# Kernel tuning notes

Hardware: AMD Instinct MI355X
Metric: run time of the kernel (lower is better)

## Reference

```python
import jax, jax.numpy as jnp
import numpy as np

B, N, E, DIN = 2048, 38, 4, 9
H0, H1, L0 = 256, 256, 512
EPS = 1e-5
_mask_np = np.ones((N, DIN), np.float32)
_mask_np[np.arange(0, N, 2), :] = 0.0
MASK = jnp.asarray(_mask_np)  # (N, DIN); masked rows zeroed


def _bn_relu(h, g, b):
    # h: (B, N, 1, D); BatchNorm2d(N) normalizes over (batch, H=1, W=D) per node channel
    mu = jnp.mean(h, axis=(0, 2, 3), keepdims=True)
    var = jnp.var(h, axis=(0, 2, 3), keepdims=True)  # biased var, as torch BN
    h = (h - mu) * jax.lax.rsqrt(var + EPS) * g[None, :, None, None] + b[None, :, None, None]
    return jax.nn.relu(h)


def _gconv(adj, nodes, Ws, bs, We, be):
    # adj: (B, E, N, N); nodes: (B, N, 1, Din)
    out = Ws.shape[0]
    hs = nodes @ Ws.T + bs  # self term: (B, N, 1, out)
    m = (nodes @ We.T + be).reshape(nodes.shape[0], N, out, E)
    hr = jnp.einsum('bemn,bnce->bmc', adj, m)  # relational aggregation
    return hs + hr[:, :, None, :]


def _forward(adj, x, cWs0, cbs0, cWe0, cbe0, cg0, cb0, cWs1, cbs1, cWe1, cbe1, cg1, cb1, lW0, lb0, lg0, lbb0, fW, fb):
    masked_x = MASK * x
    h = masked_x[:, :, None, :]
    h = _bn_relu(_gconv(adj, h, cWs0, cbs0, cWe0, cbe0), cg0, cb0)
    h = _bn_relu(_gconv(adj, h, cWs1, cbs1, cWe1, cbe1), cg1, cb1)
    h = _bn_relu(h @ lW0.T + lb0, lg0, lbb0)
    h = (h @ fW.T + fb)[:, :, 0, :]  # (B, N, 2*DIN)
    s_logits, t = h[..., :DIN], h[..., DIN:]
    s = jax.nn.sigmoid(s_logits)
    out = masked_x + (1.0 - MASK) * (x + t) * s
    logdet = jnp.sum(jax.nn.log_sigmoid(s_logits).reshape(x.shape[0], -1), axis=1)
    return out, logdet


def setup_inputs() -> dict:
    key = jax.random.key(0)
    ks = jax.random.split(key, 8)
    rn = lambda k, shape: jax.random.normal(ks[k], shape, jnp.float32) * 0.1
    return {
        'adj': jax.random.uniform(ks[0], (B, E, N, N), jnp.float32),
        'x': jax.random.normal(ks[1], (B, N, DIN), jnp.float32),
        'cWs0': rn(2, (H0, DIN)), 'cbs0': jnp.zeros((H0,), jnp.float32),
        'cWe0': rn(3, (H0 * E, DIN)), 'cbe0': jnp.zeros((H0 * E,), jnp.float32),
        'cg0': jnp.ones((N,), jnp.float32), 'cb0': jnp.zeros((N,), jnp.float32),
        'cWs1': rn(4, (H1, H0)), 'cbs1': jnp.zeros((H1,), jnp.float32),
        'cWe1': rn(5, (H1 * E, H0)), 'cbe1': jnp.zeros((H1 * E,), jnp.float32),
        'cg1': jnp.ones((N,), jnp.float32), 'cb1': jnp.zeros((N,), jnp.float32),
        'lW0': rn(6, (L0, H1)), 'lb0': jnp.zeros((L0,), jnp.float32),
        'lg0': jnp.ones((N,), jnp.float32), 'lbb0': jnp.zeros((N,), jnp.float32),
        'fW': rn(7, (2 * DIN, L0)), 'fb': jnp.zeros((2 * DIN,), jnp.float32),
    }


def reference(adj, x, cWs0, cbs0, cWe0, cbe0, cg0, cb0, cWs1, cbs1, cWe1, cbe1, cg1, cb1, lW0, lb0, lg0, lbb0, fW, fb):
    return _forward(adj, x, cWs0, cbs0, cWe0, cbe0, cg0, cb0, cWs1, cbs1, cWe1, cbe1, cg1, cb1, lW0, lb0, lg0, lbb0, fW, fb)
```

## Files before the change

kernel.cpp:

```cpp
#include <hip/hip_runtime.h>
#include <hip/hip_bf16.h>
#include <math.h>

#define B_   2048
#define N_   38
#define E_   4
#define DIN_ 9
#define H0_  256
#define H1_  256
#define L0_  512
#define M_   (B_ * N_)

typedef short bf16x8 __attribute__((ext_vector_type(8)));
typedef float f32x4 __attribute__((ext_vector_type(4)));

struct __align__(8) bf4 { __hip_bfloat16 x, y, z, w; };

__device__ __forceinline__ float b2f(unsigned short u) {
  return __uint_as_float((unsigned)u << 16);
}
__device__ __forceinline__ unsigned short f2b(float f) {
  __hip_bfloat16 h = __float2bfloat16(f);
  return *(unsigned short*)&h;
}
__device__ __forceinline__ float4 ld4v(const __hip_bfloat16* p) {
  bf4 v = *(const bf4*)p;
  return make_float4(__bfloat162float(v.x), __bfloat162float(v.y),
                     __bfloat162float(v.z), __bfloat162float(v.w));
}
__device__ __forceinline__ void st4v(__hip_bfloat16* p, float4 v) {
  bf4 o;
  o.x = __float2bfloat16(v.x); o.y = __float2bfloat16(v.y);
  o.z = __float2bfloat16(v.z); o.w = __float2bfloat16(v.w);
  *(bf4*)p = o;
}

static __device__ __forceinline__ float selc(const float4 v, int j) {
  return (j == 0) ? v.x : ((j == 1) ? v.y : ((j == 2) ? v.z : v.w));
}

__device__ __forceinline__ void fma_tile12(const float* __restrict__ zr, float4 w,
                                           float (&acc)[4][12]) {
#pragma unroll
  for (int l4 = 0; l4 < 3; ++l4) {
    float4 zv = *(const float4*)&zr[l4 * 4];
#pragma unroll
    for (int j = 0; j < 4; ++j) {
      float wj = selc(w, j);
      acc[j][l4 * 4 + 0] = fmaf(zv.x, wj, acc[j][l4 * 4 + 0]);
      acc[j][l4 * 4 + 1] = fmaf(zv.y, wj, acc[j][l4 * 4 + 1]);
      acc[j][l4 * 4 + 2] = fmaf(zv.z, wj, acc[j][l4 * 4 + 2]);
      acc[j][l4 * 4 + 3] = fmaf(zv.w, wj, acc[j][l4 * 4 + 3]);
    }
  }
}

__global__ void k_zero(float* __restrict__ p) { p[threadIdx.x] = 0.f; }

__global__ void k_build_w0(const float* __restrict__ Ws, const float* __restrict__ We,
                           float* __restrict__ WT) {
  int i = blockIdx.x * 256 + threadIdx.x;
  if (i >= 45 * 256) return;
  int r = i / 256, c = i % 256;
  float v;
  if (r < 9) v = Ws[c * 9 + r];
  else { int rr = r - 9; int e = rr / 9, f = rr % 9; v = We[(c * 4 + e) * 9 + f]; }
  WT[i] = v;
}

__global__ void k_build_wb1(const float* __restrict__ Ws, const float* __restrict__ We,
                            unsigned short* __restrict__ WT) {
  int i = blockIdx.x * 256 + threadIdx.x;
  if (i >= 256 * 1280) return;
  int c = i / 1280, k = i % 1280;
  float v;
  if (k < 256) v = Ws[c * 256 + k];
  else { int kk = k - 256; int e = kk >> 8, f = kk & 255; v = We[(c * 4 + e) * 256 + f]; }
  WT[i] = f2b(v);
}

__global__ void k_build_wl(const float* __restrict__ W, unsigned short* __restrict__ WT) {
  int i = blockIdx.x * 256 + threadIdx.x;
  if (i >= 512 * 256) return;
  WT[i] = f2b(W[i]);
}

__global__ void k_build_wf(const float* __restrict__ W, unsigned short* __restrict__ WT) {
  int i = blockIdx.x * 256 + threadIdx.x;
  if (i >= 32 * 512) return;
  int r = i / 512, k = i % 512;
  WT[i] = f2b(r < 18 ? W[r * 512 + k] : 0.f);
}

__global__ __launch_bounds__(256) void k_gconv0(
    const float* __restrict__ adj, const float* __restrict__ x,
    const float* __restrict__ WT, const float* __restrict__ bs,
    const float* __restrict__ be, __hip_bfloat16* __restrict__ g) {
  __shared__ __align__(16) float adjF[E_ * N_ * N_];
  __shared__ __align__(16) float xc[45 * 48];
  __shared__ __align__(16) float arow[E_ * 48];
  const int b = blockIdx.x, tid = threadIdx.x;
  const size_t abase = (size_t)b * (E_ * N_ * N_);
  for (int i = tid; i < E_ * N_ * N_; i += 256) adjF[i] = adj[abase + i];
  for (int i = tid; i < N_ * DIN_; i += 256) {
    int n = i / DIN_;
    float v = x[(size_t)b * (N_ * DIN_) + i];
    xc[(i % DIN_) * 48 + n] = (n & 1) ? v : 0.f;
  }
  __syncthreads();
  for (int i = tid; i < E_ * N_; i += 256) {
    int e = i / N_, m = i % N_;
    const float* ar = &adjF[(e * N_ + m) * N_];
    float s = 0.f;
    for (int n = 0; n < N_; ++n) s += ar[n];
    arow[e * 48 + m] = s;
  }
  for (int i = tid; i < 36 * N_; i += 256) {
    int m = i % N_, ef = i / N_;
    int e = ef / 9, f = ef % 9;
    const float* ar = &adjF[(e * N_ + m) * N_];
    float s = 0.f;
    for (int n = 0; n < N_; ++n) s += ar[n] * xc[f * 48 + n];
    xc[(9 + ef) * 48 + m] = s;
  }
  __syncthreads();
  const int cg = tid & 63, mg = tid >> 6;
  const int c0 = cg * 4, mb = mg * 12;
  float acc[4][12];
#pragma unroll
  for (int j = 0; j < 4; ++j) {
    float bsv = bs[c0 + j];
    float b0 = be[(c0 + j) * 4 + 0], b1 = be[(c0 + j) * 4 + 1];
    float b2 = be[(c0 + j) * 4 + 2], b3 = be[(c0 + j) * 4 + 3];
#pragma unroll
    for (int l = 0; l < 12; ++l) {
      int m = mb + l;
      acc[j][l] = bsv + arow[0 * 48 + m] * b0 + arow[1 * 48 + m] * b1 +
                  arow[2 * 48 + m] * b2 + arow[3 * 48 + m] * b3;
    }
  }
  for (int k = 0; k < 45; ++k) {
    float4 w = *(const float4*)&WT[k * 256 + c0];
    fma_tile12(&xc[k * 48 + mb], w, acc);
  }
#pragma unroll
  for (int l = 0; l < 12; ++l) {
    int m = mb + l;
    if (m < N_) {
      float4 o; o.x = acc[0][l]; o.y = acc[1][l]; o.z = acc[2][l]; o.w = acc[3][l];
      st4v(&g[((size_t)b * N_ + m) * H0_ + c0], o);
    }
  }
}

__global__ __launch_bounds__(256) void k_stats(const __hip_bfloat16* __restrict__ g, int C,
                                               float* __restrict__ st) {
  int n = blockIdx.x, s = blockIdx.y, tid = threadIdx.x;
  int C4 = C >> 2;
  float sum = 0.f, sq = 0.f;
  int per = 64 * C4;
  for (int j = tid; j < per; j += 256) {
    int bb = (s << 6) + j / C4, cc = j % C4;
    float4 v = ld4v(&g[((size_t)(bb * N_ + n) * C4 + cc) * 4]);
    sum += v.x + v.y + v.z + v.w;
    sq += v.x * v.x + v.y * v.y + v.z * v.z + v.w * v.w;
  }
  for (int off = 32; off; off >>= 1) {
    sum += __shfl_down(sum, off);
    sq += __shfl_down(sq, off);
  }
  __shared__ float rs[4], rq[4];
  int w = tid >> 6, l = tid & 63;
  if (!l) { rs[w] = sum; rq[w] = sq; }
  __syncthreads();
  if (!tid) {
    float S = 0.f, Q = 0.f;
    for (int i = 0; i < 4; ++i) { S += rs[i]; Q += rq[i]; }
    atomicAdd(&st[n * 2], S);
    atomicAdd(&st[n * 2 + 1], Q);
  }
}

#define ADJS 72
#define ZBS2 264

__global__ __launch_bounds__(512, 4) void k_gc1f(
    const float* __restrict__ adj, const unsigned short* __restrict__ g0,
    const unsigned short* __restrict__ Wb1, const float* __restrict__ bs,
    const float* __restrict__ be, const float* __restrict__ st,
    const float* __restrict__ gam, const float* __restrict__ bet,
    unsigned short* __restrict__ h2) {
  __shared__ __align__(16) unsigned short adjB[4 * 38 * ADJS];
  __shared__ __align__(16) unsigned short zB[48 * ZBS2];
  __shared__ float arowS[4 * 48];
  __shared__ float aS[40], bS[40];
  __shared__ float lbias[256];
  const int b = blockIdx.x, tid = threadIdx.x;
  for (int i = tid; i < 4 * 38 * ADJS / 8; i += 512) ((uint4*)adjB)[i] = make_uint4(0, 0, 0, 0);
  if (tid < 40) {
    int n = tid < 38 ? tid : 37;
    const float cnt = 2048.f * 256.f;
    float mu = st[n * 2] / cnt;
    float var = st[n * 2 + 1] / cnt - mu * mu;
    float a = rsqrtf(var + 1e-5f) * gam[n];
    aS[tid] = a;
    bS[tid] = bet[n] - mu * a;
  }
  if (tid >= 64 && tid < 320) lbias[tid - 64] = bs[tid - 64];
  __syncthreads();
  for (int i = tid; i < 4 * 38 * 38; i += 512) {
    int em = i / 38, n = i % 38;
    adjB[em * ADJS + n] = f2b(adj[(size_t)b * 5776 + i]);
  }
  __syncthreads();
  if (tid < 152) {
    int e = tid / 38, m = tid % 38;
    float s = 0.f;
    for (int n = 0; n < 38; ++n) s += b2f(adjB[(e * 38 + m) * ADJS + n]);
    arowS[e * 48 + m] = s;
  }
  const int w = tid >> 6, L = tid & 63;
  const int lrow = L & 15, quad = L >> 4;
  bf16x8 hfr[2][2];
#pragma unroll
  for (int ft = 0; ft < 2; ++ft) {
    const int fcol = (w * 2 + ft) * 16 + lrow;
#pragma unroll
    for (int kk = 0; kk < 2; ++kk) {
#pragma unroll
      for (int j = 0; j < 8; ++j) {
        int n = kk * 32 + quad * 8 + j;
        int nc = n < 38 ? n : 37;
        float v = b2f(g0[((size_t)b * 38 + n) * 256 + fcol]);
        v = fmaxf(fmaf(v, aS[nc], bS[nc]), 0.f);
        hfr[ft][kk][j] = (short)f2b(v);
      }
    }
  }
  f32x4 acc[3][2];
#pragma unroll
  for (int mt = 0; mt < 3; ++mt) {
    acc[mt][0] = (f32x4){0.f, 0.f, 0.f, 0.f};
    acc[mt][1] = (f32x4){0.f, 0.f, 0.f, 0.f};
  }
#pragma unroll 1
  for (int e = 0; e < 4; ++e) {
    f32x4 za[3][2];
#pragma unroll
    for (int mt = 0; mt < 3; ++mt) {
      za[mt][0] = (f32x4){0.f, 0.f, 0.f, 0.f};
      za[mt][1] = (f32x4){0.f, 0.f, 0.f, 0.f};
    }
#pragma unroll
    for (int kk = 0; kk < 2; ++kk) {
#pragma unroll
      for (int mt = 0; mt < 3; ++mt) {
        int m = mt * 16 + lrow;
        int mc = m < 38 ? m : 37;
        bf16x8 aa = *(const bf16x8*)&adjB[(e * 38 + mc) * ADJS + kk * 32 + quad * 8];
        za[mt][0] = __builtin_amdgcn_mfma_f32_16x16x32_bf16(aa, hfr[0][kk], za[mt][0], 0, 0, 0);
        za[mt][1] = __builtin_amdgcn_mfma_f32_16x16x32_bf16(aa, hfr[1][kk], za[mt][1], 0, 0, 0);
      }
    }
    __syncthreads();
#pragma unroll
    for (int mt = 0; mt < 3; ++mt)
#pragma unroll
      for (int ft = 0; ft < 2; ++ft)
#pragma unroll
        for (int reg = 0; reg < 4; ++reg)
          zB[(mt * 16 + quad * 4 + reg) * ZBS2 + (w * 2 + ft) * 16 + lrow] =
              f2b(za[mt][ft][reg]);
    __syncthreads();
    if (e == 0) {
#pragma unroll 2
      for (int kc = 0; kc < 8; ++kc) {
        bf16x8 bb0 = *(const bf16x8*)&Wb1[(size_t)(w * 32 + lrow) * 1280 + kc * 32 + quad * 8];
        bf16x8 bb1 = *(const bf16x8*)&Wb1[(size_t)(w * 32 + 16 + lrow) * 1280 + kc * 32 + quad * 8];
#pragma unroll
        for (int mt = 0; mt < 3; ++mt) {
          int m = mt * 16 + lrow;
          int mc = m < 38 ? m : 37;
          float a = aS[mc], bo = bS[mc];
          uint4 u = *(const uint4*)&g0[((size_t)b * 38 + mc) * 256 + kc * 32 + quad * 8];
          bf16x8 af;
          unsigned* up = (unsigned*)&u;
#pragma unroll
          for (int h = 0; h < 4; ++h) {
            float lo = fmaxf(fmaf(b2f((unsigned short)(up[h] & 0xffff)), a, bo), 0.f);
            float hi = fmaxf(fmaf(b2f((unsigned short)(up[h] >> 16)), a, bo), 0.f);
            af[h * 2] = (short)f2b(lo);
            af[h * 2 + 1] = (short)f2b(hi);
          }
          acc[mt][0] = __builtin_amdgcn_mfma_f32_16x16x32_bf16(af, bb0, acc[mt][0], 0, 0, 0);
          acc[mt][1] = __builtin_amdgcn_mfma_f32_16x16x32_bf16(af, bb1, acc[mt][1], 0, 0, 0);
        }
      }
    }
#pragma unroll 2
    for (int kcl = 0; kcl < 8; ++kcl) {
      const int kbase = 256 + e * 256 + kcl * 32;
      bf16x8 bb0 = *(const bf16x8*)&Wb1[(size_t)(w * 32 + lrow) * 1280 + kbase + quad * 8];
      bf16x8 bb1 = *(const bf16x8*)&Wb1[(size_t)(w * 32 + 16 + lrow) * 1280 + kbase + quad * 8];
#pragma unroll
      for (int mt = 0; mt < 3; ++mt) {
        bf16x8 af = *(const bf16x8*)&zB[(mt * 16 + lrow) * ZBS2 + kcl * 32 + quad * 8];
        acc[mt][0] = __builtin_amdgcn_mfma_f32_16x16x32_bf16(af, bb0, acc[mt][0], 0, 0, 0);
        acc[mt][1] = __builtin_amdgcn_mfma_f32_16x16x32_bf16(af, bb1, acc[mt][1], 0, 0, 0);
      }
    }
  }
#pragma unroll
  for (int mt = 0; mt < 3; ++mt) {
#pragma unroll
    for (int reg = 0; reg < 4; ++reg) {
      const int m = mt * 16 + quad * 4 + reg;
      if (m < N_) {
        float a0 = arowS[0 * 48 + m], a1 = arowS[1 * 48 + m];
        float a2 = arowS[2 * 48 + m], a3 = arowS[3 * 48 + m];
#pragma unroll
        for (int nt = 0; nt < 2; ++nt) {
          const int col = w * 32 + nt * 16 + lrow;
          float4 bev = *(const float4*)&be[col * 4];
          float v = acc[mt][nt][reg] + lbias[col] +
                    a0 * bev.x + a1 * bev.y + a2 * bev.z + a3 * bev.w;
          h2[((size_t)b * N_ + m) * 256 + col] = f2b(v);
        }
      }
    }
  }
}

__global__ __launch_bounds__(256) void k_mm(
    const unsigned short* __restrict__ A0, const unsigned short* __restrict__ Bw,
    const float* __restrict__ bias, unsigned short* __restrict__ Cout,
    int m_base, int kChunks, int sA0, int Cstride) {
  __shared__ __align__(16) unsigned short lA[64 * 32];
  __shared__ __align__(16) unsigned short lB[256 * 32];
  __shared__ float lbias[256];
  const int t = threadIdx.x;
  const int tileM = blockIdx.x, n_base = blockIdx.y * 256;
  const int K = kChunks * 32;
  for (int i = t; i < 256; i += 256) lbias[i] = bias[n_base + i];

  const int w = t >> 6, L = t & 63;
  const int lrow = L & 15, quad = L >> 4;
  const int srow = t >> 2, sseg = (t & 3) * 8;

  f32x4 acc[4][4];
#pragma unroll
  for (int mt = 0; mt < 4; ++mt)
#pragma unroll
    for (int nt = 0; nt < 4; ++nt) acc[mt][nt] = (f32x4){0.f, 0.f, 0.f, 0.f};

  for (int ki = 0; ki < kChunks; ++ki) {
    {
      const unsigned short* gp =
          A0 + (size_t)(m_base + tileM * 64 + srow) * sA0 + ki * 32 + sseg;
      __builtin_amdgcn_global_load_lds(
          (const __attribute__((address_space(1))) void*)gp,
          (__attribute__((address_space(3))) void*)(lA + w * 512), 16, 0, 0);
    }
#pragma unroll
    for (int r = 0; r < 4; ++r) {
      const unsigned short* gp = Bw + (size_t)(n_base + r * 64 + srow) * K + ki * 32 + sseg;
      __builtin_amdgcn_global_load_lds(
          (const __attribute__((address_space(1))) void*)gp,
          (__attribute__((address_space(3))) void*)(lB + r * 2048 + w * 512), 16, 0, 0);
    }
    __syncthreads();
    bf16x8 af[4], bfr[4];
#pragma unroll
    for (int mt = 0; mt < 4; ++mt)
      af[mt] = *(const bf16x8*)&lA[(mt * 16 + lrow) * 32 + quad * 8];
#pragma unroll
    for (int nt = 0; nt < 4; ++nt)
      bfr[nt] = *(const bf16x8*)&lB[(w * 64 + nt * 16 + lrow) * 32 + quad * 8];
#pragma unroll
    for (int mt = 0; mt < 4; ++mt)
#pragma unroll
      for (int nt = 0; nt < 4; ++nt)
        acc[mt][nt] = __builtin_amdgcn_mfma_f32_16x16x32_bf16(af[mt], bfr[nt], acc[mt][nt], 0, 0, 0);
    __syncthreads();
  }
#pragma unroll
  for (int mt = 0; mt < 4; ++mt) {
#pragma unroll
    for (int reg = 0; reg < 4; ++reg) {
      const size_t r_loc = (size_t)(tileM * 64 + mt * 16 + quad * 4 + reg);
#pragma unroll
      for (int nt = 0; nt < 4; ++nt) {
        const int col = w * 64 + nt * 16 + lrow;
        Cout[r_loc * Cstride + n_base + col] = f2b(acc[mt][nt][reg] + lbias[col]);
      }
    }
  }
}

__global__ __launch_bounds__(256) void k_prep2(
    unsigned short* __restrict__ g, const float* __restrict__ st,
    const float* __restrict__ gam, const float* __restrict__ bet) {
  size_t i = (size_t)blockIdx.x * 256 + threadIdx.x;
  int n = (int)((i >> 5) % N_);
  const float cnt = 2048.f * 256.f;
  float mu = st[n * 2] / cnt;
  float var = st[n * 2 + 1] / cnt - mu * mu;
  float a = rsqrtf(var + 1e-5f) * gam[n];
  float bb = bet[n] - mu * a;
  uint4 u = *((const uint4*)g + i);
  uint4 o;
  unsigned* up = (unsigned*)&u;
  unsigned* op = (unsigned*)&o;
#pragma unroll
  for (int j = 0; j < 4; ++j) {
    float lo = b2f((unsigned short)(up[j] & 0xffff));
    float hi = b2f((unsigned short)(up[j] >> 16));
    lo = fmaxf(fmaf(lo, a, bb), 0.f);
    hi = fmaxf(fmaf(hi, a, bb), 0.f);
    op[j] = (unsigned)f2b(lo) | ((unsigned)f2b(hi) << 16);
  }
  *((uint4*)g + i) = o;
}

__global__ __launch_bounds__(256) void k_final(
    const unsigned short* __restrict__ g2, const float* __restrict__ x,
    const unsigned short* __restrict__ Wfb, const float* __restrict__ fb,
    const float* __restrict__ st, const float* __restrict__ gam,
    const float* __restrict__ bet, float* __restrict__ out, int b_off) {
  __shared__ __align__(16) unsigned short hA[48 * 520];
  __shared__ float lgS[48 * 20];
  __shared__ float aS[N_], bS[N_], fbS[20], red[4];
  const int b = b_off + blockIdx.x, tid = threadIdx.x;
  const int bl = blockIdx.x;
  if (tid < N_) {
    const float cnt = 2048.f * 512.f;
    float mu = st[tid * 2] / cnt;
    float var = st[tid * 2 + 1] / cnt - mu * mu;
    float a = rsqrtf(var + 1e-5f) * gam[tid];
    aS[tid] = a;
    bS[tid] = bet[tid] - mu * a;
  }
  if (tid >= 64 && tid < 82) fbS[tid - 64] = fb[tid - 64];
  __syncthreads();
  for (int i = tid; i < N_ * 64; i += 256) {
    int n = i >> 6, seg = (i & 63) * 8;
    uint4 u = *(const uint4*)&g2[((size_t)bl * N_ + n) * 512 + seg];
    float a = aS[n], bb = bS[n];
    float v[8];
    v[0] = b2f((unsigned short)(u.x & 0xffff)); v[1] = b2f((unsigned short)(u.x >> 16));
    v[2] = b2f((unsigned short)(u.y & 0xffff)); v[3] = b2f((unsigned short)(u.y >> 16));
    v[4] = b2f((unsigned short)(u.z & 0xffff)); v[5] = b2f((unsigned short)(u.z >> 16));
    v[6] = b2f((unsigned short)(u.w & 0xffff)); v[7] = b2f((unsigned short)(u.w >> 16));
#pragma unroll
    for (int j = 0; j < 8; ++j) v[j] = fmaxf(fmaf(v[j], a, bb), 0.f);
    uint4 o;
    o.x = (unsigned)f2b(v[0]) | ((unsigned)f2b(v[1]) << 16);
    o.y = (unsigned)f2b(v[2]) | ((unsigned)f2b(v[3]) << 16);
    o.z = (unsigned)f2b(v[4]) | ((unsigned)f2b(v[5]) << 16);
    o.w = (unsigned)f2b(v[6]) | ((unsigned)f2b(v[7]) << 16);
    *(uint4*)&hA[n * 520 + seg] = o;
  }
  for (int i = tid; i < 10 * 64; i += 256) {
    int n = 38 + (i >> 6), seg = (i & 63) * 8;
    *(uint4*)&hA[n * 520 + seg] = make_uint4(0, 0, 0, 0);
  }
  __syncthreads();
  const int w = tid >> 6, L = tid & 63;
  const int lrow = L & 15, quad = L >> 4;
  if (w < 3) {
    f32x4 acc0 = (f32x4){0.f, 0.f, 0.f, 0.f}, acc1 = (f32x4){0.f, 0.f, 0.f, 0.f};
#pragma unroll
    for (int ki = 0; ki < 16; ++ki) {
      bf16x8 af = *(const bf16x8*)&hA[(w * 16 + lrow) * 520 + ki * 32 + quad * 8];
      bf16x8 b0 = *(const bf16x8*)&Wfb[(size_t)lrow * 512 + ki * 32 + quad * 8];
      bf16x8 b1 = *(const bf16x8*)&Wfb[(size_t)(16 + lrow) * 512 + ki * 32 + quad * 8];
      acc0 = __builtin_amdgcn_mfma_f32_16x16x32_bf16(af, b0, acc0, 0, 0, 0);
      acc1 = __builtin_amdgcn_mfma_f32_16x16x32_bf16(af, b1, acc1, 0, 0, 0);
    }
#pragma unroll
    for (int reg = 0; reg < 4; ++reg) {
      int m = w * 16 + quad * 4 + reg;
      if (m < N_) {
        lgS[m * 20 + lrow] = acc0[reg] + fbS[lrow];
        if (lrow < 2) lgS[m * 20 + 16 + lrow] = acc1[reg] + fbS[16 + lrow];
      }
    }
  }
  __syncthreads();
  float ls = 0.f;
  for (int ii = tid; ii < 342; ii += 256) {
    int mm = ii / 9, d = ii % 9;
    float sl = lgS[mm * 20 + d];
    float tv = lgS[mm * 20 + 9 + d];
    float xv = x[((size_t)b * N_ + mm) * 9 + d];
    float sg = 1.f / (1.f + expf(-sl));
    float o = (mm & 1) ? xv : (xv + tv) * sg;
    out[((size_t)b * N_ + mm) * 9 + d] = o;
    ls += (sl >= 0.f) ? -log1pf(expf(-sl)) : (sl - log1pf(expf(sl)));
  }
#pragma unroll
  for (int off = 32; off; off >>= 1) ls += __shfl_down(ls, off);
  if (L == 0) red[w] = ls;
  __syncthreads();
  if (tid == 0) out[(size_t)B_ * 342 + b] = red[0] + red[1] + red[2] + red[3];
}

extern "C" void kernel_launch(void* const* d_in, const int* in_sizes, int n_in,
                              void* d_out, int out_size, void* d_ws, size_t ws_size,
                              hipStream_t stream) {
  (void)in_sizes; (void)n_in; (void)out_size;
  const float* adj  = (const float*)d_in[0];
  const float* x    = (const float*)d_in[1];
  const float* cWs0 = (const float*)d_in[2];
  const float* cbs0 = (const float*)d_in[3];
  const float* cWe0 = (const float*)d_in[4];
  const float* cbe0 = (const float*)d_in[5];
  const float* cg0  = (const float*)d_in[6];
  const float* cb0  = (const float*)d_in[7];
  const float* cWs1 = (const float*)d_in[8];
  const float* cbs1 = (const float*)d_in[9];
  const float* cWe1 = (const float*)d_in[10];
  const float* cbe1 = (const float*)d_in[11];
  const float* cg1  = (const float*)d_in[12];
  const float* cb1  = (const float*)d_in[13];
  const float* lW0  = (const float*)d_in[14];
  const float* lb0  = (const float*)d_in[15];
  const float* lg0  = (const float*)d_in[16];
  const float* lbb0 = (const float*)d_in[17];
  const float* fW   = (const float*)d_in[18];
  const float* fb   = (const float*)d_in[19];
  float* out = (float*)d_out;

  char* p = (char*)d_ws;
  float* stats = (float*)p;                     p += 1024;
  float* wt0   = (float*)p;                     p += 45 * 256 * 4;
  unsigned short* Wfb = (unsigned short*)p;     p += 32 * 512 * 2;
  unsigned short* Wb1 = (unsigned short*)p;     p += 256 * 1280 * 2;
  unsigned short* Wl  = (unsigned short*)p;     p += 512 * 256 * 2;
  unsigned short* buf1 = (unsigned short*)p;    p += (size_t)M_ * 256 * 2;
  unsigned short* buf3 = (unsigned short*)p;    p += (size_t)M_ * 256 * 2;
  unsigned short* g2 = (unsigned short*)p;
  const size_t fixed = (size_t)((char*)g2 - (char*)d_ws);
  const bool full = ws_size >= fixed + (size_t)M_ * 512 * 2;

  k_zero<<<1, 256, 0, stream>>>(stats);
  k_build_w0<<<45, 256, 0, stream>>>(cWs0, cWe0, wt0);
  k_build_wb1<<<1280, 256, 0, stream>>>(cWs1, cWe1, Wb1);
  k_build_wl<<<512, 256, 0, stream>>>(lW0, Wl);
  k_build_wf<<<64, 256, 0, stream>>>(fW, Wfb);

  k_gconv0<<<2048, 256, 0, stream>>>(adj, x, wt0, cbs0, cbe0, (__hip_bfloat16*)buf1);
  k_stats<<<dim3(38, 32), 256, 0, stream>>>((const __hip_bfloat16*)buf1, 256, stats);

  k_gc1f<<<2048, 512, 0, stream>>>(adj, buf1, Wb1, cbs1, cbe1, stats, cg0, cb0, buf3);
  k_stats<<<dim3(38, 32), 256, 0, stream>>>((const __hip_bfloat16*)buf3, 256, stats + 76);

  k_prep2<<<(M_ * 256 / 8 + 255) / 256, 256, 0, stream>>>(buf3, stats + 76, cg1, cb1);

  if (full) {
    k_mm<<<dim3(M_ / 64, 2), 256, 0, stream>>>(buf3, Wl, lb0, g2, 0, 8, 256, 512);
    k_stats<<<dim3(38, 32), 256, 0, stream>>>((const __hip_bfloat16*)g2, 512, stats + 152);
    k_final<<<2048, 256, 0, stream>>>(g2, x, Wfb, fb, stats + 152, lg0, lbb0, out, 0);
  } else {
    for (int h = 0; h < 2; ++h) {
      k_mm<<<dim3(M_ / 128, 2), 256, 0, stream>>>(buf3, Wl, lb0, g2, h * (M_ / 2), 8, 256, 512);
      k_stats<<<dim3(38, 16), 256, 0, stream>>>((const __hip_bfloat16*)g2, 512, stats + 152);
    }
    for (int h = 0; h < 2; ++h) {
      k_mm<<<dim3(M_ / 128, 2), 256, 0, stream>>>(buf3, Wl, lb0, g2, h * (M_ / 2), 8, 256, 512);
      k_final<<<1024, 256, 0, stream>>>(g2, x, Wfb, fb, stats + 152, lg0, lbb0, out, h * 1024);
    }
  }
}
```

Measured before the change: 540.1 us.

## Reorder layer-1 gconv as feature GEMM first, then per-batch adjacency aggregation

Replaces the fused per-batch gconv1 kernel, which aggregated adjacency times h and then multiplied by the weights, with a large dense GEMM that first projects the normalized features onto a combined weight matrix (self plus 4 edge blocks, 1280 outputs). A separate kernel then multiplies the adjacency by the projected features per edge type and adds the self term and biases. BN-ReLU on layer 0 now runs as a separate in-place pass, and the linear layer uses a new 128x256 tile GEMM with 512 threads. The change also drops the fallback for a small workspace, so it assumes enough workspace for the 1280-wide intermediate. That intermediate adds global memory traffic in exchange for better MFMA utilization.

```diff
diff --git a/kernel.cpp b/kernel.cpp
--- a/kernel.cpp
+++ b/kernel.cpp
@@ -68,14 +68,14 @@
   WT[i] = v;
 }
 
-__global__ void k_build_wb1(const float* __restrict__ Ws, const float* __restrict__ We,
-                            unsigned short* __restrict__ WT) {
+__global__ void k_build_wbig(const float* __restrict__ Ws, const float* __restrict__ We,
+                             unsigned short* __restrict__ WT) {
   int i = blockIdx.x * 256 + threadIdx.x;
-  if (i >= 256 * 1280) return;
-  int c = i / 1280, k = i % 1280;
+  if (i >= 1280 * 256) return;
+  int j = i / 256, f = i % 256;
   float v;
-  if (k < 256) v = Ws[c * 256 + k];
-  else { int kk = k - 256; int e = kk >> 8, f = kk & 255; v = We[(c * 4 + e) * 256 + f]; }
+  if (j < 256) v = Ws[j * 256 + f];
+  else { int jj = j - 256; int e = jj >> 8, c = jj & 255; v = We[(c * 4 + e) * 256 + f]; }
   WT[i] = f2b(v);
 }
 
@@ -181,222 +181,6 @@
   }
 }
 
-#define ADJS 72
-#define ZBS2 264
-
-__global__ __launch_bounds__(512, 4) void k_gc1f(
-    const float* __restrict__ adj, const unsigned short* __restrict__ g0,
-    const unsigned short* __restrict__ Wb1, const float* __restrict__ bs,
-    const float* __restrict__ be, const float* __restrict__ st,
-    const float* __restrict__ gam, const float* __restrict__ bet,
-    unsigned short* __restrict__ h2) {
-  __shared__ __align__(16) unsigned short adjB[4 * 38 * ADJS];
-  __shared__ __align__(16) unsigned short zB[48 * ZBS2];
-  __shared__ float arowS[4 * 48];
-  __shared__ float aS[40], bS[40];
-  __shared__ float lbias[256];
-  const int b = blockIdx.x, tid = threadIdx.x;
-  for (int i = tid; i < 4 * 38 * ADJS / 8; i += 512) ((uint4*)adjB)[i] = make_uint4(0, 0, 0, 0);
-  if (tid < 40) {
-    int n = tid < 38 ? tid : 37;
-    const float cnt = 2048.f * 256.f;
-    float mu = st[n * 2] / cnt;
-    float var = st[n * 2 + 1] / cnt - mu * mu;
-    float a = rsqrtf(var + 1e-5f) * gam[n];
-    aS[tid] = a;
-    bS[tid] = bet[n] - mu * a;
-  }
-  if (tid >= 64 && tid < 320) lbias[tid - 64] = bs[tid - 64];
-  __syncthreads();
-  for (int i = tid; i < 4 * 38 * 38; i += 512) {
-    int em = i / 38, n = i % 38;
-    adjB[em * ADJS + n] = f2b(adj[(size_t)b * 5776 + i]);
-  }
-  __syncthreads();
-  if (tid < 152) {
-    int e = tid / 38, m = tid % 38;
-    float s = 0.f;
-    for (int n = 0; n < 38; ++n) s += b2f(adjB[(e * 38 + m) * ADJS + n]);
-    arowS[e * 48 + m] = s;
-  }
-  const int w = tid >> 6, L = tid & 63;
-  const int lrow = L & 15, quad = L >> 4;
-  bf16x8 hfr[2][2];
-#pragma unroll
-  for (int ft = 0; ft < 2; ++ft) {
-    const int fcol = (w * 2 + ft) * 16 + lrow;
-#pragma unroll
-    for (int kk = 0; kk < 2; ++kk) {
-#pragma unroll
-      for (int j = 0; j < 8; ++j) {
-        int n = kk * 32 + quad * 8 + j;
-        int nc = n < 38 ? n : 37;
-        float v = b2f(g0[((size_t)b * 38 + n) * 256 + fcol]);
-        v = fmaxf(fmaf(v, aS[nc], bS[nc]), 0.f);
-        hfr[ft][kk][j] = (short)f2b(v);
-      }
-    }
-  }
-  f32x4 acc[3][2];
-#pragma unroll
-  for (int mt = 0; mt < 3; ++mt) {
-    acc[mt][0] = (f32x4){0.f, 0.f, 0.f, 0.f};
-    acc[mt][1] = (f32x4){0.f, 0.f, 0.f, 0.f};
-  }
-#pragma unroll 1
-  for (int e = 0; e < 4; ++e) {
-    f32x4 za[3][2];
-#pragma unroll
-    for (int mt = 0; mt < 3; ++mt) {
-      za[mt][0] = (f32x4){0.f, 0.f, 0.f, 0.f};
-      za[mt][1] = (f32x4){0.f, 0.f, 0.f, 0.f};
-    }
-#pragma unroll
-    for (int kk = 0; kk < 2; ++kk) {
-#pragma unroll
-      for (int mt = 0; mt < 3; ++mt) {
-        int m = mt * 16 + lrow;
-        int mc = m < 38 ? m : 37;
-        bf16x8 aa = *(const bf16x8*)&adjB[(e * 38 + mc) * ADJS + kk * 32 + quad * 8];
-        za[mt][0] = __builtin_amdgcn_mfma_f32_16x16x32_bf16(aa, hfr[0][kk], za[mt][0], 0, 0, 0);
-        za[mt][1] = __builtin_amdgcn_mfma_f32_16x16x32_bf16(aa, hfr[1][kk], za[mt][1], 0, 0, 0);
-      }
-    }
-    __syncthreads();
-#pragma unroll
-    for (int mt = 0; mt < 3; ++mt)
-#pragma unroll
-      for (int ft = 0; ft < 2; ++ft)
-#pragma unroll
-        for (int reg = 0; reg < 4; ++reg)
-          zB[(mt * 16 + quad * 4 + reg) * ZBS2 + (w * 2 + ft) * 16 + lrow] =
-              f2b(za[mt][ft][reg]);
-    __syncthreads();
-    if (e == 0) {
-#pragma unroll 2
-      for (int kc = 0; kc < 8; ++kc) {
-        bf16x8 bb0 = *(const bf16x8*)&Wb1[(size_t)(w * 32 + lrow) * 1280 + kc * 32 + quad * 8];
-        bf16x8 bb1 = *(const bf16x8*)&Wb1[(size_t)(w * 32 + 16 + lrow) * 1280 + kc * 32 + quad * 8];
-#pragma unroll
-        for (int mt = 0; mt < 3; ++mt) {
-          int m = mt * 16 + lrow;
-          int mc = m < 38 ? m : 37;
-          float a = aS[mc], bo = bS[mc];
-          uint4 u = *(const uint4*)&g0[((size_t)b * 38 + mc) * 256 + kc * 32 + quad * 8];
-          bf16x8 af;
-          unsigned* up = (unsigned*)&u;
-#pragma unroll
-          for (int h = 0; h < 4; ++h) {
-            float lo = fmaxf(fmaf(b2f((unsigned short)(up[h] & 0xffff)), a, bo), 0.f);
-            float hi = fmaxf(fmaf(b2f((unsigned short)(up[h] >> 16)), a, bo), 0.f);
-            af[h * 2] = (short)f2b(lo);
-            af[h * 2 + 1] = (short)f2b(hi);
-          }
-          acc[mt][0] = __builtin_amdgcn_mfma_f32_16x16x32_bf16(af, bb0, acc[mt][0], 0, 0, 0);
-          acc[mt][1] = __builtin_amdgcn_mfma_f32_16x16x32_bf16(af, bb1, acc[mt][1], 0, 0, 0);
-        }
-      }
-    }
-#pragma unroll 2
-    for (int kcl = 0; kcl < 8; ++kcl) {
-      const int kbase = 256 + e * 256 + kcl * 32;
-      bf16x8 bb0 = *(const bf16x8*)&Wb1[(size_t)(w * 32 + lrow) * 1280 + kbase + quad * 8];
-      bf16x8 bb1 = *(const bf16x8*)&Wb1[(size_t)(w * 32 + 16 + lrow) * 1280 + kbase + quad * 8];
-#pragma unroll
-      for (int mt = 0; mt < 3; ++mt) {
-        bf16x8 af = *(const bf16x8*)&zB[(mt * 16 + lrow) * ZBS2 + kcl * 32 + quad * 8];
-        acc[mt][0] = __builtin_amdgcn_mfma_f32_16x16x32_bf16(af, bb0, acc[mt][0], 0, 0, 0);
-        acc[mt][1] = __builtin_amdgcn_mfma_f32_16x16x32_bf16(af, bb1, acc[mt][1], 0, 0, 0);
-      }
-    }
-  }
-#pragma unroll
-  for (int mt = 0; mt < 3; ++mt) {
-#pragma unroll
-    for (int reg = 0; reg < 4; ++reg) {
-      const int m = mt * 16 + quad * 4 + reg;
-      if (m < N_) {
-        float a0 = arowS[0 * 48 + m], a1 = arowS[1 * 48 + m];
-        float a2 = arowS[2 * 48 + m], a3 = arowS[3 * 48 + m];
-#pragma unroll
-        for (int nt = 0; nt < 2; ++nt) {
-          const int col = w * 32 + nt * 16 + lrow;
-          float4 bev = *(const float4*)&be[col * 4];
-          float v = acc[mt][nt][reg] + lbias[col] +
-                    a0 * bev.x + a1 * bev.y + a2 * bev.z + a3 * bev.w;
-          h2[((size_t)b * N_ + m) * 256 + col] = f2b(v);
-        }
-      }
-    }
-  }
-}
-
-__global__ __launch_bounds__(256) void k_mm(
-    const unsigned short* __restrict__ A0, const unsigned short* __restrict__ Bw,
-    const float* __restrict__ bias, unsigned short* __restrict__ Cout,
-    int m_base, int kChunks, int sA0, int Cstride) {
-  __shared__ __align__(16) unsigned short lA[64 * 32];
-  __shared__ __align__(16) unsigned short lB[256 * 32];
-  __shared__ float lbias[256];
-  const int t = threadIdx.x;
-  const int tileM = blockIdx.x, n_base = blockIdx.y * 256;
-  const int K = kChunks * 32;
-  for (int i = t; i < 256; i += 256) lbias[i] = bias[n_base + i];
-
-  const int w = t >> 6, L = t & 63;
-  const int lrow = L & 15, quad = L >> 4;
-  const int srow = t >> 2, sseg = (t & 3) * 8;
-
-  f32x4 acc[4][4];
-#pragma unroll
-  for (int mt = 0; mt < 4; ++mt)
-#pragma unroll
-    for (int nt = 0; nt < 4; ++nt) acc[mt][nt] = (f32x4){0.f, 0.f, 0.f, 0.f};
-
-  for (int ki = 0; ki < kChunks; ++ki) {
-    {
-      const unsigned short* gp =
-          A0 + (size_t)(m_base + tileM * 64 + srow) * sA0 + ki * 32 + sseg;
-      __builtin_amdgcn_global_load_lds(
-          (const __attribute__((address_space(1))) void*)gp,
-          (__attribute__((address_space(3))) void*)(lA + w * 512), 16, 0, 0);
-    }
-#pragma unroll
-    for (int r = 0; r < 4; ++r) {
-      const unsigned short* gp = Bw + (size_t)(n_base + r * 64 + srow) * K + ki * 32 + sseg;
-      __builtin_amdgcn_global_load_lds(
-          (const __attribute__((address_space(1))) void*)gp,
-          (__attribute__((address_space(3))) void*)(lB + r * 2048 + w * 512), 16, 0, 0);
-    }
-    __syncthreads();
-    bf16x8 af[4], bfr[4];
-#pragma unroll
-    for (int mt = 0; mt < 4; ++mt)
-      af[mt] = *(const bf16x8*)&lA[(mt * 16 + lrow) * 32 + quad * 8];
-#pragma unroll
-    for (int nt = 0; nt < 4; ++nt)
-      bfr[nt] = *(const bf16x8*)&lB[(w * 64 + nt * 16 + lrow) * 32 + quad * 8];
-#pragma unroll
-    for (int mt = 0; mt < 4; ++mt)
-#pragma unroll
-      for (int nt = 0; nt < 4; ++nt)
-        acc[mt][nt] = __builtin_amdgcn_mfma_f32_16x16x32_bf16(af[mt], bfr[nt], acc[mt][nt], 0, 0, 0);
-    __syncthreads();
-  }
-#pragma unroll
-  for (int mt = 0; mt < 4; ++mt) {
-#pragma unroll
-    for (int reg = 0; reg < 4; ++reg) {
-      const size_t r_loc = (size_t)(tileM * 64 + mt * 16 + quad * 4 + reg);
-#pragma unroll
-      for (int nt = 0; nt < 4; ++nt) {
-        const int col = w * 64 + nt * 16 + lrow;
-        Cout[r_loc * Cstride + n_base + col] = f2b(acc[mt][nt][reg] + lbias[col]);
-      }
-    }
-  }
-}
-
 __global__ __launch_bounds__(256) void k_prep2(
     unsigned short* __restrict__ g, const float* __restrict__ st,
     const float* __restrict__ gam, const float* __restrict__ bet) {
@@ -422,16 +206,158 @@
   *((uint4*)g + i) = o;
 }
 
+template <bool BIAS>
+__global__ __launch_bounds__(512) void k_gemm(
+    const unsigned short* __restrict__ A0, const unsigned short* __restrict__ Bw,
+    const float* __restrict__ bias, unsigned short* __restrict__ Cout,
+    int Cstride) {
+  __shared__ __align__(16) unsigned short lA[128 * 32];
+  __shared__ __align__(16) unsigned short lB[256 * 32];
+  __shared__ float lbias[256];
+  const int t = threadIdx.x;
+  const int tileM = blockIdx.x, n_base = blockIdx.y * 256;
+  if (BIAS && t < 256) lbias[t] = bias[n_base + t];
+  const int w = t >> 6, L = t & 63;
+  const int wr = w >> 2, wc = w & 3;
+  const int lrow = L & 15, quad = L >> 4;
+  const int srow = t >> 2, sseg = (t & 3) * 8;
+  f32x4 acc[4][4];
+#pragma unroll
+  for (int mt = 0; mt < 4; ++mt)
+#pragma unroll
+    for (int nt = 0; nt < 4; ++nt) acc[mt][nt] = (f32x4){0.f, 0.f, 0.f, 0.f};
+
+  for (int ki = 0; ki < 8; ++ki) {
+    {
+      const unsigned short* gp = A0 + (size_t)(tileM * 128 + srow) * 256 + ki * 32 + sseg;
+      __builtin_amdgcn_global_load_lds(
+          (const __attribute__((address_space(1))) void*)gp,
+          (__attribute__((address_space(3))) void*)(lA + w * 512), 16, 0, 0);
+    }
+#pragma unroll
+    for (int r = 0; r < 2; ++r) {
+      const unsigned short* gp = Bw + (size_t)(n_base + r * 128 + srow) * 256 + ki * 32 + sseg;
+      __builtin_amdgcn_global_load_lds(
+          (const __attribute__((address_space(1))) void*)gp,
+          (__attribute__((address_space(3))) void*)(lB + r * 4096 + w * 512), 16, 0, 0);
+    }
+    __syncthreads();
+    bf16x8 af[4], bfr[4];
+#pragma unroll
+    for (int mt = 0; mt < 4; ++mt)
+      af[mt] = *(const bf16x8*)&lA[(wr * 64 + mt * 16 + lrow) * 32 + quad * 8];
+#pragma unroll
+    for (int nt = 0; nt < 4; ++nt)
+      bfr[nt] = *(const bf16x8*)&lB[(wc * 64 + nt * 16 + lrow) * 32 + quad * 8];
+#pragma unroll
+    for (int mt = 0; mt < 4; ++mt)
+#pragma unroll
+      for (int nt = 0; nt < 4; ++nt)
+        acc[mt][nt] = __builtin_amdgcn_mfma_f32_16x16x32_bf16(af[mt], bfr[nt], acc[mt][nt], 0, 0, 0);
+    __syncthreads();
+  }
+#pragma unroll
+  for (int mt = 0; mt < 4; ++mt) {
+#pragma unroll
+    for (int reg = 0; reg < 4; ++reg) {
+      const size_t row = (size_t)tileM * 128 + wr * 64 + mt * 16 + quad * 4 + reg;
+#pragma unroll
+      for (int nt = 0; nt < 4; ++nt) {
+        const int lcol = wc * 64 + nt * 16 + lrow;
+        float v = acc[mt][nt][reg];
+        if (BIAS) v += lbias[lcol];
+        Cout[row * Cstride + n_base + lcol] = f2b(v);
+      }
+    }
+  }
+}
+
+__global__ __launch_bounds__(256) void k_hr(
+    const float* __restrict__ adj, const unsigned short* __restrict__ Y,
+    const float* __restrict__ bs, const float* __restrict__ be,
+    unsigned short* __restrict__ h2, int b_base) {
+  __shared__ __align__(16) unsigned short adjE[4 * 48 * 64];
+  __shared__ __align__(16) unsigned short Ybt[256 * 72];
+  __shared__ float arowS[4 * 48];
+  const int t = threadIdx.x;
+  const int bl = blockIdx.x, b = b_base + bl;
+  for (int i = t; i < 4 * 48 * 64 / 8; i += 256) ((uint4*)adjE)[i] = make_uint4(0, 0, 0, 0);
+#pragma unroll
+  for (int n = 38; n < 64; ++n) Ybt[t * 72 + n] = 0;
+  __syncthreads();
+  for (int i = t; i < 4 * 38 * 38; i += 256) {
+    int e = i / 1444, r = i % 1444, m = r / 38, n = r % 38;
+    adjE[(e * 48 + m) * 64 + n] = f2b(adj[(size_t)b * 5776 + i]);
+  }
+  __syncthreads();
+  if (t < 152) {
+    int e = t / 38, m = t % 38;
+    float s = 0.f;
+    for (int n = 0; n < 38; ++n) s += b2f(adjE[(e * 48 + m) * 64 + n]);
+    arowS[e * 48 + m] = s;
+  }
+  const int w = t >> 6, L = t & 63;
+  const int lrow = L & 15, quad = L >> 4;
+  f32x4 acc[3][4];
+#pragma unroll
+  for (int mt = 0; mt < 3; ++mt)
+#pragma unroll
+    for (int nt = 0; nt < 4; ++nt) acc[mt][nt] = (f32x4){0.f, 0.f, 0.f, 0.f};
+#pragma unroll 1
+  for (int e = 0; e < 4; ++e) {
+    __syncthreads();
+    {
+      const unsigned short* yp = Y + (size_t)bl * 38 * 1280 + 256 + e * 256 + t;
+#pragma unroll
+      for (int n = 0; n < 38; ++n) Ybt[t * 72 + n] = yp[(size_t)n * 1280];
+    }
+    __syncthreads();
+#pragma unroll
+    for (int kk = 0; kk < 2; ++kk) {
+      bf16x8 bb[4];
+#pragma unroll
+      for (int nt = 0; nt < 4; ++nt)
+        bb[nt] = *(const bf16x8*)&Ybt[(w * 64 + nt * 16 + lrow) * 72 + kk * 32 + quad * 8];
+#pragma unroll
+      for (int mt = 0; mt < 3; ++mt) {
+        bf16x8 aa = *(const bf16x8*)&adjE[(e * 48 + mt * 16 + lrow) * 64 + kk * 32 + quad * 8];
+#pragma unroll
+        for (int nt = 0; nt < 4; ++nt)
+          acc[mt][nt] = __builtin_amdgcn_mfma_f32_16x16x32_bf16(aa, bb[nt], acc[mt][nt], 0, 0, 0);
+      }
+    }
+  }
+#pragma unroll
+  for (int mt = 0; mt < 3; ++mt) {
+#pragma unroll
+    for (int reg = 0; reg < 4; ++reg) {
+      const int m = mt * 16 + quad * 4 + reg;
+      if (m < N_) {
+        float a0 = arowS[0 * 48 + m], a1 = arowS[1 * 48 + m];
+        float a2 = arowS[2 * 48 + m], a3 = arowS[3 * 48 + m];
+#pragma unroll
+        for (int nt = 0; nt < 4; ++nt) {
+          const int col = w * 64 + nt * 16 + lrow;
+          float hs = b2f(Y[(size_t)(bl * 38 + m) * 1280 + col]);
+          float4 bev = *(const float4*)&be[col * 4];
+          float v = acc[mt][nt][reg] + hs + bs[col] +
+                    a0 * bev.x + a1 * bev.y + a2 * bev.z + a3 * bev.w;
+          h2[((size_t)b * N_ + m) * 256 + col] = f2b(v);
+        }
+      }
+    }
+  }
+}
+
 __global__ __launch_bounds__(256) void k_final(
     const unsigned short* __restrict__ g2, const float* __restrict__ x,
     const unsigned short* __restrict__ Wfb, const float* __restrict__ fb,
     const float* __restrict__ st, const float* __restrict__ gam,
-    const float* __restrict__ bet, float* __restrict__ out, int b_off) {
+    const float* __restrict__ bet, float* __restrict__ out) {
   __shared__ __align__(16) unsigned short hA[48 * 520];
   __shared__ float lgS[48 * 20];
   __shared__ float aS[N_], bS[N_], fbS[20], red[4];
-  const int b = b_off + blockIdx.x, tid = threadIdx.x;
-  const int bl = blockIdx.x;
+  const int b = blockIdx.x, tid = threadIdx.x;
   if (tid < N_) {
     const float cnt = 2048.f * 512.f;
     float mu = st[tid * 2] / cnt;
@@ -444,7 +370,7 @@
   __syncthreads();
   for (int i = tid; i < N_ * 64; i += 256) {
     int n = i >> 6, seg = (i & 63) * 8;
-    uint4 u = *(const uint4*)&g2[((size_t)bl * N_ + n) * 512 + seg];
+    uint4 u = *(const uint4*)&g2[((size_t)b * N_ + n) * 512 + seg];
     float a = aS[n], bb = bS[n];
     float v[8];
     v[0] = b2f((unsigned short)(u.x & 0xffff)); v[1] = b2f((unsigned short)(u.x >> 16));
@@ -508,7 +434,7 @@
 extern "C" void kernel_launch(void* const* d_in, const int* in_sizes, int n_in,
                               void* d_out, int out_size, void* d_ws, size_t ws_size,
                               hipStream_t stream) {
-  (void)in_sizes; (void)n_in; (void)out_size;
+  (void)in_sizes; (void)n_in; (void)out_size; (void)ws_size;
   const float* adj  = (const float*)d_in[0];
   const float* x    = (const float*)d_in[1];
   const float* cWs0 = (const float*)d_in[2];
@@ -534,41 +460,35 @@
   char* p = (char*)d_ws;
   float* stats = (float*)p;                     p += 1024;
   float* wt0   = (float*)p;                     p += 45 * 256 * 4;
-  unsigned short* Wfb = (unsigned short*)p;     p += 32 * 512 * 2;
-  unsigned short* Wb1 = (unsigned short*)p;     p += 256 * 1280 * 2;
-  unsigned short* Wl  = (unsigned short*)p;     p += 512 * 256 * 2;
-  unsigned short* buf1 = (unsigned short*)p;    p += (size_t)M_ * 256 * 2;
-  unsigned short* buf3 = (unsigned short*)p;    p += (size_t)M_ * 256 * 2;
-  unsigned short* g2 = (unsigned short*)p;
-  const size_t fixed = (size_t)((char*)g2 - (char*)d_ws);
-  const bool full = ws_size >= fixed + (size_t)M_ * 512 * 2;
+  unsigned short* Wfb  = (unsigned short*)p;    p += 32 * 512 * 2;
+  unsigned short* Wbig = (unsigned short*)p;    p += 1280 * 256 * 2;
+  unsigned short* Wl   = (unsigned short*)p;    p += 512 * 256 * 2;
+  unsigned short* g0   = (unsigned short*)p;    p += (size_t)M_ * 256 * 2;
+  unsigned short* h2   = (unsigned short*)p;    p += (size_t)M_ * 256 * 2;
+  unsigned short* big  = (unsigned short*)p;
+  unsigned short* Ybuf = big;
+  unsigned short* g2   = big;
 
   k_zero<<<1, 256, 0, stream>>>(stats);
   k_build_w0<<<45, 256, 0, stream>>>(cWs0, cWe0, wt0);
-  k_build_wb1<<<1280, 256, 0, stream>>>(cWs1, cWe1, Wb1);
+  k_build_wbig<<<1280, 256, 0, stream>>>(cWs1, cWe1, Wbig);
   k_build_wl<<<512, 256, 0, stream>>>(lW0, Wl);
   k_build_wf<<<64, 256, 0, stream>>>(fW, Wfb);
 
-  k_gconv0<<<2048, 256, 0, stream>>>(adj, x, wt0, cbs0, cbe0, (__hip_bfloat16*)buf1);
-  k_stats<<<dim3(38, 32), 256, 0, stream>>>((const __hip_bfloat16*)buf1, 256, stats);
-
-  k_gc1f<<<2048, 512, 0, stream>>>(adj, buf1, Wb1, cbs1, cbe1, stats, cg0, cb0, buf3);
-  k_stats<<<dim3(38, 32), 256, 0, stream>>>((const __hip_bfloat16*)buf3, 256, stats + 76);
-
-  k_prep2<<<(M_ * 256 / 8 + 255) / 256, 256, 0, stream>>>(buf3, stats + 76, cg1, cb1);
-
-  if (full) {
-    k_mm<<<dim3(M_ / 64, 2), 256, 0, stream>>>(buf3, Wl, lb0, g2, 0, 8, 256, 512);
-    k_stats<<<dim3(38, 32), 256, 0, stream>>>((const __hip_bfloat16*)g2, 512, stats + 152);
-    k_final<<<2048, 256, 0, stream>>>(g2, x, Wfb, fb, stats + 152, lg0, lbb0, out, 0);
-  } else {
-    for (int h = 0; h < 2; ++h) {
-      k_mm<<<dim3(M_ / 128, 2), 256, 0, stream>>>(buf3, Wl, lb0, g2, h * (M_ / 2), 8, 256, 512);
-      k_stats<<<dim3(38, 16), 256, 0, stream>>>((const __hip_bfloat16*)g2, 512, stats + 152);
-    }
-    for (int h = 0; h < 2; ++h) {
-      k_mm<<<dim3(M_ / 128, 2), 256, 0, stream>>>(buf3, Wl, lb0, g2, h * (M_ / 2), 8, 256, 512);
-      k_final<<<1024, 256, 0, stream>>>(g2, x, Wfb, fb, stats + 152, lg0, lbb0, out, h * 1024);
-    }
-  }
-}
+  k_gconv0<<<2048, 256, 0, stream>>>(adj, x, wt0, cbs0, cbe0, (__hip_bfloat16*)g0);
+  k_stats<<<dim3(38, 32), 256, 0, stream>>>((const __hip_bfloat16*)g0, 256, stats);
+  k_prep2<<<M_ * 256 / 8 / 256, 256, 0, stream>>>(g0, stats, cg0, cb0);
+
+  for (int hh = 0; hh < 2; ++hh) {
+    k_gemm<false><<<dim3(304, 5), 512, 0, stream>>>(
+        g0 + (size_t)hh * (M_ / 2) * 256, Wbig, (const float*)nullptr, Ybuf, 1280);
+    k_hr<<<1024, 256, 0, stream>>>(adj, Ybuf, cbs1, cbe1, h2, hh * 1024);
+  }
+  k_stats<<<dim3(38, 32), 256, 0, stream>>>((const __hip_bfloat16*)h2, 256, stats + 76);
+  k_prep2<<<M_ * 256 / 8 / 256, 256, 0, stream>>>(h2, stats + 76, cg1, cb1);
+
+  k_gemm<true><<<dim3(608, 2), 512, 0, stream>>>(h2, Wl, lb0, g2, 512);
+  k_stats<<<dim3(38, 32), 256, 0, stream>>>((const __hip_bfloat16*)g2, 512, stats + 152);
+
+  k_final<<<2048, 256, 0, stream>>>(g2, x, Wfb, fb, stats + 152, lg0, lbb0, out);
+}
```

Measured after the change: 516.8 us. 1.05x faster.
